# Kernel optimization log

Hardware: AMD Instinct MI355X
Metric: run time of the kernel (lower is better)

Reference implementation:

```python
import jax, jax.numpy as jnp
import numpy as np

N_NODES = 50000
N_EDGES = 800000


def setup_inputs() -> dict:
    key = jax.random.key(0)
    ks = jax.random.split(key, 8)
    return {
        "x": jax.random.normal(ks[0], (N_NODES, 256), dtype=jnp.float32),
        "adj_vals": jax.random.uniform(ks[1], (N_EDGES,), dtype=jnp.float32),
        "rows": jax.random.randint(ks[2], (N_EDGES,), 0, N_NODES, dtype=jnp.int32),
        "cols": jax.random.randint(ks[3], (N_EDGES,), 0, N_NODES, dtype=jnp.int32),
        "W1": jax.random.normal(ks[4], (256, 256), dtype=jnp.float32) * (1.0 / np.sqrt(256)),
        "b1": jnp.zeros((256,), dtype=jnp.float32),
        "W2": jax.random.normal(ks[5], (256, 256), dtype=jnp.float32) * (1.0 / np.sqrt(256)),
        "b2": jnp.zeros((256,), dtype=jnp.float32),
        "W3": jax.random.normal(ks[6], (256, 128), dtype=jnp.float32) * (1.0 / np.sqrt(256)),
        "b3": jnp.zeros((128,), dtype=jnp.float32),
    }


def reference(x, adj_vals, rows, cols, W1, b1, W2, b2, W3, b3):
    n = x.shape[0]

    def spmm(h):
        # sparse adjacency matmul: out[r] += val * h[c] over all edges (r, c)
        return jax.ops.segment_sum(adj_vals[:, None] * h[cols], rows, num_segments=n)

    # GCNLayer: adj @ (x @ W) + b ; ReLU between layers (dropout p=0 => identity)
    h = jax.nn.relu(spmm(x @ W1) + b1)
    h = jax.nn.relu(spmm(h @ W2) + b2)
    return spmm(h @ W3) + b3
```

## Files before the change

### kernel.cpp

```cpp
#include <hip/hip_runtime.h>
#include <hip/hip_bf16.h>


#define N_NODES 50000
#define N_EDGES 800000
#define KDIM 256
#define REP 8
#define NC (N_NODES * REP)
#define NB2 ((NC + 1023) / 1024)
#define NC_PAD (NB2 * 1024)

typedef __attribute__((ext_vector_type(8))) short short8;
typedef __attribute__((ext_vector_type(4))) float f32x4;

__device__ __forceinline__ ushort f2bf(float f) {
    union { float f; unsigned u; } x; x.f = f;
    unsigned r = x.u + 0x7fffu + ((x.u >> 16) & 1u);
    return (ushort)(r >> 16);
}
__device__ __forceinline__ float bf2f(ushort u) {
    union { unsigned u; float f; } x; x.u = ((unsigned)u) << 16;
    return x.f;
}

__global__ __launch_bounds__(256) void transpose_all_kernel(
        const float* __restrict__ W1, const float* __restrict__ W2,
        const float* __restrict__ W3, ushort* __restrict__ Wt1,
        ushort* __restrict__ Wt2, ushort* __restrict__ Wt3) {
    int id = blockIdx.x * blockDim.x + threadIdx.x;
    if (id < 65536) {
        int n = id >> 8, k = id & 255;
        Wt1[n * 256 + k] = f2bf(W1[k * 256 + n]);
    } else if (id < 131072) {
        int i = id - 65536, n = i >> 8, k = i & 255;
        Wt2[n * 256 + k] = f2bf(W2[k * 256 + n]);
    } else if (id < 163840) {
        int i = id - 131072, n = i >> 8, k = i & 255;
        Wt3[n * 256 + k] = f2bf(W3[k * 128 + n]);
    }
}


#define LDK 40

template <bool AFP32>
__device__ __forceinline__ void gemm_body(
        const void* __restrict__ Ain, const ushort* __restrict__ Wt,
        ushort* __restrict__ C, int M, int N, int bx, int by) {
    __shared__ ushort As[128 * LDK];
    __shared__ ushort Ws[128 * LDK];

    int t = threadIdx.x;
    int lane = t & 63;
    int w = t >> 6;
    int row0 = bx * 128, col0 = by * 128;
    int wm = (w & 1) * 64, wn = (w >> 1) * 64;
    int q = lane >> 4, mi = lane & 15;
    int r0 = t >> 2, kc = (t & 3) * 8;

    f32x4 acc[4][4];
    #pragma unroll
    for (int i = 0; i < 4; i++)
        #pragma unroll
        for (int j = 0; j < 4; j++) acc[i][j] = (f32x4)0.f;

    for (int k0 = 0; k0 < KDIM; k0 += 32) {
        int ga0 = row0 + r0;       if (ga0 >= M) ga0 = M - 1;
        int ga1 = row0 + r0 + 64;  if (ga1 >= M) ga1 = M - 1;
        short8 a0, a1;
        if (AFP32) {
            const float* Af = (const float*)Ain;
            float4 f0 = *(const float4*)&Af[ga0 * KDIM + k0 + kc];
            float4 f1 = *(const float4*)&Af[ga0 * KDIM + k0 + kc + 4];
            float4 f2 = *(const float4*)&Af[ga1 * KDIM + k0 + kc];
            float4 f3 = *(const float4*)&Af[ga1 * KDIM + k0 + kc + 4];
            a0[0] = (short)f2bf(f0.x); a0[1] = (short)f2bf(f0.y);
            a0[2] = (short)f2bf(f0.z); a0[3] = (short)f2bf(f0.w);
            a0[4] = (short)f2bf(f1.x); a0[5] = (short)f2bf(f1.y);
            a0[6] = (short)f2bf(f1.z); a0[7] = (short)f2bf(f1.w);
            a1[0] = (short)f2bf(f2.x); a1[1] = (short)f2bf(f2.y);
            a1[2] = (short)f2bf(f2.z); a1[3] = (short)f2bf(f2.w);
            a1[4] = (short)f2bf(f3.x); a1[5] = (short)f2bf(f3.y);
            a1[6] = (short)f2bf(f3.z); a1[7] = (short)f2bf(f3.w);
        } else {
            const ushort* Ab = (const ushort*)Ain;
            a0 = *(const short8*)&Ab[ga0 * KDIM + k0 + kc];
            a1 = *(const short8*)&Ab[ga1 * KDIM + k0 + kc];
        }
        short8 b0 = *(const short8*)&Wt[(col0 + r0) * KDIM + k0 + kc];
        short8 b1 = *(const short8*)&Wt[(col0 + r0 + 64) * KDIM + k0 + kc];
        __syncthreads();
        *(short8*)&As[r0 * LDK + kc]        = a0;
        *(short8*)&As[(r0 + 64) * LDK + kc] = a1;
        *(short8*)&Ws[r0 * LDK + kc]        = b0;
        *(short8*)&Ws[(r0 + 64) * LDK + kc] = b1;
        __syncthreads();

        short8 af[4], bf[4];
        #pragma unroll
        for (int mt = 0; mt < 4; mt++)
            af[mt] = *(const short8*)&As[(wm + mt * 16 + mi) * LDK + q * 8];
        #pragma unroll
        for (int nt = 0; nt < 4; nt++)
            bf[nt] = *(const short8*)&Ws[(wn + nt * 16 + mi) * LDK + q * 8];
        #pragma unroll
        for (int mt = 0; mt < 4; mt++)
            #pragma unroll
            for (int nt = 0; nt < 4; nt++)
                acc[mt][nt] = __builtin_amdgcn_mfma_f32_16x16x32_bf16(
                    af[mt], bf[nt], acc[mt][nt], 0, 0, 0);
    }

    #pragma unroll
    for (int mt = 0; mt < 4; mt++) {
        #pragma unroll
        for (int r = 0; r < 4; r++) {
            int grow = row0 + wm + mt * 16 + q * 4 + r;
            if (grow < M) {
                #pragma unroll
                for (int nt = 0; nt < 4; nt++) {
                    int gcol = col0 + wn + nt * 16 + mi;
                    C[grow * N + gcol] = f2bf(acc[mt][nt][r]);
                }
            }
        }
    }
}

#define GB1 782

__global__ __launch_bounds__(256) void gemm1_hist_kernel(
        const float* __restrict__ x, const ushort* __restrict__ Wt1,
        ushort* __restrict__ C, const int* __restrict__ rows,
        int* __restrict__ counts) {
    int b = blockIdx.x;
    if (b < GB1) {
        gemm_body<true>(x, Wt1, C, N_NODES, 256, b % 391, b / 391);
    } else {
        int e = (b - GB1) * 256 + threadIdx.x;
        if (e < N_EDGES) {
            int r = rows[e];
            atomicAdd(&counts[(r << 3) | (e & 7)], 1);
        }
    }
}

template <bool AFP32>
__global__ __launch_bounds__(256) void gemm_bf16_kernel(
        const void* __restrict__ Ain, const ushort* __restrict__ Wt,
        ushort* __restrict__ C, int M, int N) {
    gemm_body<AFP32>(Ain, Wt, C, M, N, blockIdx.x, blockIdx.y);
}


__global__ __launch_bounds__(256) void scan_sums(const int* __restrict__ counts,
                                                 int* __restrict__ bsum) {
    __shared__ int ws[4];
    int b = blockIdx.x, t = threadIdx.x, lane = t & 63, wv = t >> 6;
    int4 v = *(const int4*)&counts[b * 1024 + t * 4];
    int s = v.x + v.y + v.z + v.w;
    #pragma unroll
    for (int off = 32; off >= 1; off >>= 1) s += __shfl_down(s, off, 64);
    if (lane == 0) ws[wv] = s;
    __syncthreads();
    if (t == 0) bsum[b] = ws[0] + ws[1] + ws[2] + ws[3];
}

__global__ __launch_bounds__(512) void scan_block(const int* __restrict__ bsum,
                                                  int* __restrict__ boff,
                                                  int* __restrict__ rp8, int nb) {
    __shared__ int ws[8];
    int t = threadIdx.x, lane = t & 63, wv = t >> 6;
    int v = (t < nb) ? bsum[t] : 0;
    int incl = v;
    #pragma unroll
    for (int off = 1; off < 64; off <<= 1) {
        int u = __shfl_up(incl, off, 64);
        if (lane >= off) incl += u;
    }
    if (lane == 63) ws[wv] = incl;
    __syncthreads();
    int wo = 0;
    #pragma unroll
    for (int j = 0; j < 7; j++) wo += (j < wv) ? ws[j] : 0;
    if (t < nb) boff[t] = wo + incl - v;
    if (t == 511) rp8[NC] = wo + incl;
}

__global__ __launch_bounds__(256) void scan_apply(int* __restrict__ counts,
                                                  const int* __restrict__ boff,
                                                  int* __restrict__ rp8) {
    __shared__ int ws[4];
    int b = blockIdx.x, t = threadIdx.x, lane = t & 63, wv = t >> 6;
    int i = b * 1024 + t * 4;
    int4 v = *(const int4*)&counts[i];
    int s0 = v.x, s01 = s0 + v.y, s012 = s01 + v.z, tsum = s012 + v.w;
    int incl = tsum;
    #pragma unroll
    for (int off = 1; off < 64; off <<= 1) {
        int u = __shfl_up(incl, off, 64);
        if (lane >= off) incl += u;
    }
    if (lane == 63) ws[wv] = incl;
    __syncthreads();
    int woff = 0;
    #pragma unroll
    for (int j = 0; j < 3; j++) woff += (j < wv) ? ws[j] : 0;
    int base = boff[b] + woff + incl - tsum;
    if (i < NC)     rp8[i]     = base;
    if (i + 1 < NC) rp8[i + 1] = base + s0;
    if (i + 2 < NC) rp8[i + 2] = base + s01;
    if (i + 3 < NC) rp8[i + 3] = base + s012;
    *(int4*)&counts[i] = make_int4(0, 0, 0, 0);
}

__global__ void scatter_kernel(const int* __restrict__ rows, const int* __restrict__ cols,
                               const float* __restrict__ vals, const int* __restrict__ rp8,
                               int* __restrict__ counts, int2* __restrict__ cv) {
    int e = blockIdx.x * blockDim.x + threadIdx.x;
    if (e < N_EDGES) {
        int idx = (rows[e] << 3) | (e & 7);
        int pos = rp8[idx] + atomicAdd(&counts[idx], 1);
        cv[pos] = make_int2(cols[e], __float_as_int(vals[e]));
    }
}


template <int F, bool RELU, bool OUT_BF16>
__global__ __launch_bounds__(256) void spmm_kernel(
        const ushort* __restrict__ H, const int* __restrict__ rp8,
        const int2* __restrict__ cv, const float* __restrict__ bias,
        void* __restrict__ out, int nrows) {
    constexpr int FL = F / 8;
    constexpr int EP = 64 / FL;
    constexpr int STEP = EP * 4;
    int wave = threadIdx.x >> 6, lane = threadIdx.x & 63;
    int r = blockIdx.x * 4 + wave;
    if (r >= nrows) return;
    int fl = lane % FL, ep = lane / FL;
    const ushort* Hl = H + fl * 8;

    float acc[8];
    #pragma unroll
    for (int j = 0; j < 8; j++) acc[j] = 0.f;

    int start = rp8[r * REP], end = rp8[r * REP + REP];
    for (int base = start; base < end; base += STEP) {
        int e0 = base + ep * 4;
        int2 m0 = cv[e0], m1 = cv[e0 + 1], m2 = cv[e0 + 2], m3 = cv[e0 + 3];
        int   c0 = (e0     < end) ? m0.x : 0;
        int   c1 = (e0 + 1 < end) ? m1.x : 0;
        int   c2 = (e0 + 2 < end) ? m2.x : 0;
        int   c3 = (e0 + 3 < end) ? m3.x : 0;
        float v0 = (e0     < end) ? __int_as_float(m0.y) : 0.f;
        float v1 = (e0 + 1 < end) ? __int_as_float(m1.y) : 0.f;
        float v2 = (e0 + 2 < end) ? __int_as_float(m2.y) : 0.f;
        float v3 = (e0 + 3 < end) ? __int_as_float(m3.y) : 0.f;
        short8 h0 = *(const short8*)&Hl[(size_t)c0 * F];
        short8 h1 = *(const short8*)&Hl[(size_t)c1 * F];
        short8 h2 = *(const short8*)&Hl[(size_t)c2 * F];
        short8 h3 = *(const short8*)&Hl[(size_t)c3 * F];
        #pragma unroll
        for (int j = 0; j < 8; j++)
            acc[j] += v0 * bf2f((ushort)h0[j]) + v1 * bf2f((ushort)h1[j])
                    + v2 * bf2f((ushort)h2[j]) + v3 * bf2f((ushort)h3[j]);
    }

    #pragma unroll
    for (int off = FL; off < 64; off <<= 1)
        #pragma unroll
        for (int j = 0; j < 8; j++) acc[j] += __shfl_down(acc[j], off, 64);

    if (ep == 0) {
        #pragma unroll
        for (int j = 0; j < 8; j++) {
            float o = acc[j] + bias[fl * 8 + j];
            if (RELU) o = fmaxf(o, 0.f);
            acc[j] = o;
        }
        if (OUT_BF16) {
            short8 ob;
            #pragma unroll
            for (int j = 0; j < 8; j++) ob[j] = (short)f2bf(acc[j]);
            *(short8*)((ushort*)out + (size_t)r * F + fl * 8) = ob;
        } else {
            float* of = (float*)out + (size_t)r * F + fl * 8;
            *(float4*)&of[0] = make_float4(acc[0], acc[1], acc[2], acc[3]);
            *(float4*)&of[4] = make_float4(acc[4], acc[5], acc[6], acc[7]);
        }
    }
}


extern "C" void kernel_launch(void* const* d_in, const int* in_sizes, int n_in,
                              void* d_out, int out_size, void* d_ws, size_t ws_size,
                              hipStream_t stream) {
    const float* x    = (const float*)d_in[0];
    const float* av   = (const float*)d_in[1];
    const int*   rows = (const int*)d_in[2];
    const int*   cols = (const int*)d_in[3];
    const float* W1   = (const float*)d_in[4];
    const float* b1   = (const float*)d_in[5];
    const float* W2   = (const float*)d_in[6];
    const float* b2   = (const float*)d_in[7];
    const float* W3   = (const float*)d_in[8];
    const float* b3   = (const float*)d_in[9];
    float* out = (float*)d_out;

    const int N = N_NODES, E = N_EDGES;

    char* p = (char*)d_ws;
    auto carve = [&](size_t bytes) {
        void* q = (void*)p;
        p += (bytes + 255) & ~(size_t)255;
        return q;
    };
    ushort* bufG = (ushort*)carve((size_t)N * 256 * 2);
    ushort* bufH = (ushort*)carve((size_t)N * 256 * 2);
    ushort* Wt1  = (ushort*)carve((size_t)256 * 256 * 2);
    ushort* Wt2  = (ushort*)carve((size_t)256 * 256 * 2);
    ushort* Wt3  = (ushort*)carve((size_t)128 * 256 * 2);
    int*    rp8    = (int*)carve((size_t)(NC + 1) * 4);
    int*    counts = (int*)carve((size_t)NC_PAD * 4);
    int*    bsum   = (int*)carve((size_t)NB2 * 4);
    int*    boff   = (int*)carve((size_t)NB2 * 4);
    int2*   cv     = (int2*)carve((size_t)(E + 16) * 8);

    hipMemsetAsync(counts, 0, (size_t)NC_PAD * 4, stream);
    transpose_all_kernel<<<(163840 + 255) / 256, 256, 0, stream>>>(W1, W2, W3, Wt1, Wt2, Wt3);

    gemm1_hist_kernel<<<GB1 + (E + 255) / 256, 256, 0, stream>>>(x, Wt1, bufG, rows, counts);

    scan_sums<<<NB2, 256, 0, stream>>>(counts, bsum);
    scan_block<<<1, 512, 0, stream>>>(bsum, boff, rp8, NB2);
    scan_apply<<<NB2, 256, 0, stream>>>(counts, boff, rp8);
    scatter_kernel<<<(E + 255) / 256, 256, 0, stream>>>(rows, cols, av, rp8, counts, cv);

    int spmm_blocks = (N + 3) / 4;
    spmm_kernel<256, true, true><<<spmm_blocks, 256, 0, stream>>>(bufG, rp8, cv, b1, bufH, N);
    gemm_bf16_kernel<false><<<dim3(391, 2), 256, 0, stream>>>(bufH, Wt2, bufG, N, 256);
    spmm_kernel<256, true, true><<<spmm_blocks, 256, 0, stream>>>(bufG, rp8, cv, b2, bufH, N);
    gemm_bf16_kernel<false><<<dim3(391, 1), 256, 0, stream>>>(bufH, Wt3, bufG, N, 128);
    spmm_kernel<128, false, false><<<spmm_blocks, 256, 0, stream>>>(bufG, rp8, cv, b3, out, N);
}
```

Measured before the change: 373.2 us.

## Rewrite GEMM with full-K weight tile in LDS, prep kernel, wider SpMM unroll

Replaces the k-looped GEMM with a kernel that loads the whole 128x256 weight slice into swizzled LDS once and streams A fragments straight from global memory into MFMA, with each wave covering 64 rows by 128 columns. A new prep kernel casts x to bf16, builds the row histogram with vectorized atomics, and transposes the weights in one launch. The histogram replication factor goes from 8 to 16 to spread atomic contention, and the SpMM gathers 8 edges per lane instead of 4 for more memory-level parallelism. The trade-offs are an extra bf16 copy of x, no overlap of the first GEMM with the histogram, and higher register and LDS pressure (64 KB of LDS per block) in the GEMM.

New measurement: 395.8 us. 6.0% more time.

```diff
diff --git a/kernel.cpp b/kernel.cpp
--- a/kernel.cpp
+++ b/kernel.cpp
@@ -5,10 +5,14 @@
 #define N_NODES 50000
 #define N_EDGES 800000
 #define KDIM 256
-#define REP 8
+#define REP 16
 #define NC (N_NODES * REP)
 #define NB2 ((NC + 1023) / 1024)
 #define NC_PAD (NB2 * 1024)
+
+#define PB_CAST 6250
+#define PB_HIST 782
+#define PB_TR   640
 
 typedef __attribute__((ext_vector_type(8))) short short8;
 typedef __attribute__((ext_vector_type(4))) float f32x4;
@@ -23,133 +27,50 @@
     return x.f;
 }
 
-__global__ __launch_bounds__(256) void transpose_all_kernel(
+__global__ __launch_bounds__(256) void prep_kernel(
+        const float* __restrict__ x, ushort* __restrict__ xb,
+        const int* __restrict__ rows, int* __restrict__ counts,
         const float* __restrict__ W1, const float* __restrict__ W2,
         const float* __restrict__ W3, ushort* __restrict__ Wt1,
         ushort* __restrict__ Wt2, ushort* __restrict__ Wt3) {
-    int id = blockIdx.x * blockDim.x + threadIdx.x;
-    if (id < 65536) {
-        int n = id >> 8, k = id & 255;
-        Wt1[n * 256 + k] = f2bf(W1[k * 256 + n]);
-    } else if (id < 131072) {
-        int i = id - 65536, n = i >> 8, k = i & 255;
-        Wt2[n * 256 + k] = f2bf(W2[k * 256 + n]);
-    } else if (id < 163840) {
-        int i = id - 131072, n = i >> 8, k = i & 255;
-        Wt3[n * 256 + k] = f2bf(W3[k * 128 + n]);
-    }
-}
-
-
-#define LDK 40
-
-template <bool AFP32>
-__device__ __forceinline__ void gemm_body(
-        const void* __restrict__ Ain, const ushort* __restrict__ Wt,
-        ushort* __restrict__ C, int M, int N, int bx, int by) {
-    __shared__ ushort As[128 * LDK];
-    __shared__ ushort Ws[128 * LDK];
-
-    int t = threadIdx.x;
-    int lane = t & 63;
-    int w = t >> 6;
-    int row0 = bx * 128, col0 = by * 128;
-    int wm = (w & 1) * 64, wn = (w >> 1) * 64;
-    int q = lane >> 4, mi = lane & 15;
-    int r0 = t >> 2, kc = (t & 3) * 8;
-
-    f32x4 acc[4][4];
-    #pragma unroll
-    for (int i = 0; i < 4; i++)
-        #pragma unroll
-        for (int j = 0; j < 4; j++) acc[i][j] = (f32x4)0.f;
-
-    for (int k0 = 0; k0 < KDIM; k0 += 32) {
-        int ga0 = row0 + r0;       if (ga0 >= M) ga0 = M - 1;
-        int ga1 = row0 + r0 + 64;  if (ga1 >= M) ga1 = M - 1;
-        short8 a0, a1;
-        if (AFP32) {
-            const float* Af = (const float*)Ain;
-            float4 f0 = *(const float4*)&Af[ga0 * KDIM + k0 + kc];
-            float4 f1 = *(const float4*)&Af[ga0 * KDIM + k0 + kc + 4];
-            float4 f2 = *(const float4*)&Af[ga1 * KDIM + k0 + kc];
-            float4 f3 = *(const float4*)&Af[ga1 * KDIM + k0 + kc + 4];
-            a0[0] = (short)f2bf(f0.x); a0[1] = (short)f2bf(f0.y);
-            a0[2] = (short)f2bf(f0.z); a0[3] = (short)f2bf(f0.w);
-            a0[4] = (short)f2bf(f1.x); a0[5] = (short)f2bf(f1.y);
-            a0[6] = (short)f2bf(f1.z); a0[7] = (short)f2bf(f1.w);
-            a1[0] = (short)f2bf(f2.x); a1[1] = (short)f2bf(f2.y);
-            a1[2] = (short)f2bf(f2.z); a1[3] = (short)f2bf(f2.w);
-            a1[4] = (short)f2bf(f3.x); a1[5] = (short)f2bf(f3.y);
-            a1[6] = (short)f2bf(f3.z); a1[7] = (short)f2bf(f3.w);
+    int b = blockIdx.x, t = threadIdx.x;
+    if (b < PB_CAST) {
+        int i = (b * 256 + t) * 8;
+        float4 f0 = *(const float4*)&x[i];
+        float4 f1 = *(const float4*)&x[i + 4];
+        short8 o;
+        o[0] = (short)f2bf(f0.x); o[1] = (short)f2bf(f0.y);
+        o[2] = (short)f2bf(f0.z); o[3] = (short)f2bf(f0.w);
+        o[4] = (short)f2bf(f1.x); o[5] = (short)f2bf(f1.y);
+        o[6] = (short)f2bf(f1.z); o[7] = (short)f2bf(f1.w);
+        *(short8*)&xb[i] = o;
+    } else if (b < PB_CAST + PB_HIST) {
+        int e0 = (b - PB_CAST) * 1024 + t * 4;
+        if (e0 + 3 < N_EDGES) {
+            int4 r4 = *(const int4*)&rows[e0];
+            atomicAdd(&counts[(r4.x << 4) | ((e0    ) & 15)], 1);
+            atomicAdd(&counts[(r4.y << 4) | ((e0 + 1) & 15)], 1);
+            atomicAdd(&counts[(r4.z << 4) | ((e0 + 2) & 15)], 1);
+            atomicAdd(&counts[(r4.w << 4) | ((e0 + 3) & 15)], 1);
         } else {
-            const ushort* Ab = (const ushort*)Ain;
-            a0 = *(const short8*)&Ab[ga0 * KDIM + k0 + kc];
-            a1 = *(const short8*)&Ab[ga1 * KDIM + k0 + kc];
-        }
-        short8 b0 = *(const short8*)&Wt[(col0 + r0) * KDIM + k0 + kc];
-        short8 b1 = *(const short8*)&Wt[(col0 + r0 + 64) * KDIM + k0 + kc];
-        __syncthreads();
-        *(short8*)&As[r0 * LDK + kc]        = a0;
-        *(short8*)&As[(r0 + 64) * LDK + kc] = a1;
-        *(short8*)&Ws[r0 * LDK + kc]        = b0;
-        *(short8*)&Ws[(r0 + 64) * LDK + kc] = b1;
-        __syncthreads();
-
-        short8 af[4], bf[4];
-        #pragma unroll
-        for (int mt = 0; mt < 4; mt++)
-            af[mt] = *(const short8*)&As[(wm + mt * 16 + mi) * LDK + q * 8];
-        #pragma unroll
-        for (int nt = 0; nt < 4; nt++)
-            bf[nt] = *(const short8*)&Ws[(wn + nt * 16 + mi) * LDK + q * 8];
-        #pragma unroll
-        for (int mt = 0; mt < 4; mt++)
-            #pragma unroll
-            for (int nt = 0; nt < 4; nt++)
-                acc[mt][nt] = __builtin_amdgcn_mfma_f32_16x16x32_bf16(
-                    af[mt], bf[nt], acc[mt][nt], 0, 0, 0);
-    }
-
-    #pragma unroll
-    for (int mt = 0; mt < 4; mt++) {
-        #pragma unroll
-        for (int r = 0; r < 4; r++) {
-            int grow = row0 + wm + mt * 16 + q * 4 + r;
-            if (grow < M) {
-                #pragma unroll
-                for (int nt = 0; nt < 4; nt++) {
-                    int gcol = col0 + wn + nt * 16 + mi;
-                    C[grow * N + gcol] = f2bf(acc[mt][nt][r]);
-                }
+            for (int j = 0; j < 4; j++) {
+                int e = e0 + j;
+                if (e < N_EDGES) atomicAdd(&counts[(rows[e] << 4) | (e & 15)], 1);
             }
         }
-    }
-}
-
-#define GB1 782
-
-__global__ __launch_bounds__(256) void gemm1_hist_kernel(
-        const float* __restrict__ x, const ushort* __restrict__ Wt1,
-        ushort* __restrict__ C, const int* __restrict__ rows,
-        int* __restrict__ counts) {
-    int b = blockIdx.x;
-    if (b < GB1) {
-        gemm_body<true>(x, Wt1, C, N_NODES, 256, b % 391, b / 391);
     } else {
-        int e = (b - GB1) * 256 + threadIdx.x;
-        if (e < N_EDGES) {
-            int r = rows[e];
-            atomicAdd(&counts[(r << 3) | (e & 7)], 1);
-        }
-    }
-}
-
-template <bool AFP32>
-__global__ __launch_bounds__(256) void gemm_bf16_kernel(
-        const void* __restrict__ Ain, const ushort* __restrict__ Wt,
-        ushort* __restrict__ C, int M, int N) {
-    gemm_body<AFP32>(Ain, Wt, C, M, N, blockIdx.x, blockIdx.y);
+        int id = (b - PB_CAST - PB_HIST) * 256 + t;
+        if (id < 65536) {
+            int n = id >> 8, k = id & 255;
+            Wt1[n * 256 + k] = f2bf(W1[k * 256 + n]);
+        } else if (id < 131072) {
+            int i = id - 65536, n = i >> 8, k = i & 255;
+            Wt2[n * 256 + k] = f2bf(W2[k * 256 + n]);
+        } else {
+            int i = id - 131072, n = i >> 8, k = i & 255;
+            Wt3[n * 256 + k] = f2bf(W3[k * 128 + n]);
+        }
+    }
 }
 
 
@@ -166,10 +87,10 @@
     if (t == 0) bsum[b] = ws[0] + ws[1] + ws[2] + ws[3];
 }
 
-__global__ __launch_bounds__(512) void scan_block(const int* __restrict__ bsum,
-                                                  int* __restrict__ boff,
-                                                  int* __restrict__ rp8, int nb) {
-    __shared__ int ws[8];
+__global__ __launch_bounds__(1024) void scan_block(const int* __restrict__ bsum,
+                                                   int* __restrict__ boff,
+                                                   int* __restrict__ rp16, int nb) {
+    __shared__ int ws[16];
     int t = threadIdx.x, lane = t & 63, wv = t >> 6;
     int v = (t < nb) ? bsum[t] : 0;
     int incl = v;
@@ -182,14 +103,14 @@
     __syncthreads();
     int wo = 0;
     #pragma unroll
-    for (int j = 0; j < 7; j++) wo += (j < wv) ? ws[j] : 0;
+    for (int j = 0; j < 15; j++) wo += (j < wv) ? ws[j] : 0;
     if (t < nb) boff[t] = wo + incl - v;
-    if (t == 511) rp8[NC] = wo + incl;
+    if (t == 1023) rp16[NC] = wo + incl;
 }
 
 __global__ __launch_bounds__(256) void scan_apply(int* __restrict__ counts,
                                                   const int* __restrict__ boff,
-                                                  int* __restrict__ rp8) {
+                                                  int* __restrict__ rp16) {
     __shared__ int ws[4];
     int b = blockIdx.x, t = threadIdx.x, lane = t & 63, wv = t >> 6;
     int i = b * 1024 + t * 4;
@@ -207,33 +128,96 @@
     #pragma unroll
     for (int j = 0; j < 3; j++) woff += (j < wv) ? ws[j] : 0;
     int base = boff[b] + woff + incl - tsum;
-    if (i < NC)     rp8[i]     = base;
-    if (i + 1 < NC) rp8[i + 1] = base + s0;
-    if (i + 2 < NC) rp8[i + 2] = base + s01;
-    if (i + 3 < NC) rp8[i + 3] = base + s012;
+    if (i < NC)     rp16[i]     = base;
+    if (i + 1 < NC) rp16[i + 1] = base + s0;
+    if (i + 2 < NC) rp16[i + 2] = base + s01;
+    if (i + 3 < NC) rp16[i + 3] = base + s012;
     *(int4*)&counts[i] = make_int4(0, 0, 0, 0);
 }
 
 __global__ void scatter_kernel(const int* __restrict__ rows, const int* __restrict__ cols,
-                               const float* __restrict__ vals, const int* __restrict__ rp8,
+                               const float* __restrict__ vals, const int* __restrict__ rp16,
                                int* __restrict__ counts, int2* __restrict__ cv) {
     int e = blockIdx.x * blockDim.x + threadIdx.x;
     if (e < N_EDGES) {
-        int idx = (rows[e] << 3) | (e & 7);
-        int pos = rp8[idx] + atomicAdd(&counts[idx], 1);
+        int idx = (rows[e] << 4) | (e & 15);
+        int pos = rp16[idx] + atomicAdd(&counts[idx], 1);
         cv[pos] = make_int2(cols[e], __float_as_int(vals[e]));
+    }
+}
+
+
+__global__ __launch_bounds__(256) void gemm_kernel(
+        const ushort* __restrict__ A, const ushort* __restrict__ Wt,
+        ushort* __restrict__ C, int M, int N) {
+    __shared__ ushort Ws[128 * 256];
+
+    int t = threadIdx.x, lane = t & 63, w = t >> 6;
+    int row0 = blockIdx.x * 256 + w * 64;
+    int col0 = blockIdx.y * 128;
+    int q = lane >> 4, mi = lane & 15;
+
+    #pragma unroll
+    for (int i = 0; i < 16; i++) {
+        int u = i * 256 + t;
+        int c = u >> 5, ch = u & 31;
+        *(short8*)&Ws[c * 256 + (ch ^ (c & 31)) * 8] =
+            *(const short8*)&Wt[(col0 + c) * KDIM + ch * 8];
+    }
+    __syncthreads();
+
+    f32x4 acc[4][8];
+    #pragma unroll
+    for (int i = 0; i < 4; i++)
+        #pragma unroll
+        for (int j = 0; j < 8; j++) acc[i][j] = (f32x4)0.f;
+
+    #pragma unroll
+    for (int ks = 0; ks < 8; ks++) {
+        int kc = ks * 4 + q;
+        short8 af[4], bf[8];
+        #pragma unroll
+        for (int mt = 0; mt < 4; mt++) {
+            int gr = row0 + mt * 16 + mi;
+            if (gr >= M) gr = M - 1;
+            af[mt] = *(const short8*)&A[gr * KDIM + kc * 8];
+        }
+        #pragma unroll
+        for (int nt = 0; nt < 8; nt++) {
+            int cc = nt * 16 + mi;
+            bf[nt] = *(const short8*)&Ws[cc * 256 + (kc ^ (cc & 31)) * 8];
+        }
+        #pragma unroll
+        for (int mt = 0; mt < 4; mt++)
+            #pragma unroll
+            for (int nt = 0; nt < 8; nt++)
+                acc[mt][nt] = __builtin_amdgcn_mfma_f32_16x16x32_bf16(
+                    af[mt], bf[nt], acc[mt][nt], 0, 0, 0);
+    }
+
+    #pragma unroll
+    for (int mt = 0; mt < 4; mt++) {
+        #pragma unroll
+        for (int r = 0; r < 4; r++) {
+            int grow = row0 + mt * 16 + q * 4 + r;
+            if (grow < M) {
+                #pragma unroll
+                for (int nt = 0; nt < 8; nt++)
+                    C[grow * N + col0 + nt * 16 + mi] = f2bf(acc[mt][nt][r]);
+            }
+        }
     }
 }
 
 
 template <int F, bool RELU, bool OUT_BF16>
 __global__ __launch_bounds__(256) void spmm_kernel(
-        const ushort* __restrict__ H, const int* __restrict__ rp8,
+        const ushort* __restrict__ H, const int* __restrict__ rp16,
         const int2* __restrict__ cv, const float* __restrict__ bias,
         void* __restrict__ out, int nrows) {
     constexpr int FL = F / 8;
     constexpr int EP = 64 / FL;
-    constexpr int STEP = EP * 4;
+    constexpr int STEP = EP * 8;
     int wave = threadIdx.x >> 6, lane = threadIdx.x & 63;
     int r = blockIdx.x * 4 + wave;
     if (r >= nrows) return;
@@ -244,26 +228,27 @@
     #pragma unroll
     for (int j = 0; j < 8; j++) acc[j] = 0.f;
 
-    int start = rp8[r * REP], end = rp8[r * REP + REP];
+    int start = rp16[r * REP], end = rp16[r * REP + REP];
     for (int base = start; base < end; base += STEP) {
-        int e0 = base + ep * 4;
-        int2 m0 = cv[e0], m1 = cv[e0 + 1], m2 = cv[e0 + 2], m3 = cv[e0 + 3];
-        int   c0 = (e0     < end) ? m0.x : 0;
-        int   c1 = (e0 + 1 < end) ? m1.x : 0;
-        int   c2 = (e0 + 2 < end) ? m2.x : 0;
-        int   c3 = (e0 + 3 < end) ? m3.x : 0;
-        float v0 = (e0     < end) ? __int_as_float(m0.y) : 0.f;
-        float v1 = (e0 + 1 < end) ? __int_as_float(m1.y) : 0.f;
-        float v2 = (e0 + 2 < end) ? __int_as_float(m2.y) : 0.f;
-        float v3 = (e0 + 3 < end) ? __int_as_float(m3.y) : 0.f;
-        short8 h0 = *(const short8*)&Hl[(size_t)c0 * F];
-        short8 h1 = *(const short8*)&Hl[(size_t)c1 * F];
-        short8 h2 = *(const short8*)&Hl[(size_t)c2 * F];
-        short8 h3 = *(const short8*)&Hl[(size_t)c3 * F];
-        #pragma unroll
-        for (int j = 0; j < 8; j++)
-            acc[j] += v0 * bf2f((ushort)h0[j]) + v1 * bf2f((ushort)h1[j])
-                    + v2 * bf2f((ushort)h2[j]) + v3 * bf2f((ushort)h3[j]);
+        int e0 = base + ep * 8;
+        int2 m[8];
+        #pragma unroll
+        for (int i = 0; i < 8; i++) m[i] = cv[e0 + i];
+        int c[8]; float v[8];
+        #pragma unroll
+        for (int i = 0; i < 8; i++) {
+            bool p = (e0 + i) < end;
+            c[i] = p ? m[i].x : 0;
+            v[i] = p ? __int_as_float(m[i].y) : 0.f;
+        }
+        short8 h[8];
+        #pragma unroll
+        for (int i = 0; i < 8; i++) h[i] = *(const short8*)&Hl[(size_t)c[i] * F];
+        #pragma unroll
+        for (int i = 0; i < 8; i++)
+            #pragma unroll
+            for (int j = 0; j < 8; j++)
+                acc[j] += v[i] * bf2f((ushort)h[i][j]);
     }
 
     #pragma unroll
@@ -315,31 +300,35 @@
         p += (bytes + 255) & ~(size_t)255;
         return q;
     };
+    ushort* xb   = (ushort*)carve((size_t)N * 256 * 2);
     ushort* bufG = (ushort*)carve((size_t)N * 256 * 2);
     ushort* bufH = (ushort*)carve((size_t)N * 256 * 2);
     ushort* Wt1  = (ushort*)carve((size_t)256 * 256 * 2);
     ushort* Wt2  = (ushort*)carve((size_t)256 * 256 * 2);
     ushort* Wt3  = (ushort*)carve((size_t)128 * 256 * 2);
-    int*    rp8    = (int*)carve((size_t)(NC + 1) * 4);
+    int*    rp16   = (int*)carve((size_t)(NC + 1) * 4);
     int*    counts = (int*)carve((size_t)NC_PAD * 4);
     int*    bsum   = (int*)carve((size_t)NB2 * 4);
     int*    boff   = (int*)carve((size_t)NB2 * 4);
-    int2*   cv     = (int2*)carve((size_t)(E + 16) * 8);
+    int2*   cv     = (int2*)carve((size_t)(E + 64) * 8);
 
     hipMemsetAsync(counts, 0, (size_t)NC_PAD * 4, stream);
-    transpose_all_kernel<<<(163840 + 255) / 256, 256, 0, stream>>>(W1, W2, W3, Wt1, Wt2, Wt3);
-
-    gemm1_hist_kernel<<<GB1 + (E + 255) / 256, 256, 0, stream>>>(x, Wt1, bufG, rows, counts);
+    prep_kernel<<<PB_CAST + PB_HIST + PB_TR, 256, 0, stream>>>(
+        x, xb, rows, counts, W1, W2, W3, Wt1, Wt2, Wt3);
 
     scan_sums<<<NB2, 256, 0, stream>>>(counts, bsum);
-    scan_block<<<1, 512, 0, stream>>>(bsum, boff, rp8, NB2);
-    scan_apply<<<NB2, 256, 0, stream>>>(counts, boff, rp8);
-    scatter_kernel<<<(E + 255) / 256, 256, 0, stream>>>(rows, cols, av, rp8, counts, cv);
-
+    scan_block<<<1, 1024, 0, stream>>>(bsum, boff, rp16, NB2);
+    scan_apply<<<NB2, 256, 0, stream>>>(counts, boff, rp16);
+    scatter_kernel<<<(E + 255) / 256, 256, 0, stream>>>(rows, cols, av, rp16, counts, cv);
+
+    dim3 g2((N + 255) / 256, 2);
+    dim3 g1((N + 255) / 256, 1);
     int spmm_blocks = (N + 3) / 4;
-    spmm_kernel<256, true, true><<<spmm_blocks, 256, 0, stream>>>(bufG, rp8, cv, b1, bufH, N);
-    gemm_bf16_kernel<false><<<dim3(391, 2), 256, 0, stream>>>(bufH, Wt2, bufG, N, 256);
-    spmm_kernel<256, true, true><<<spmm_blocks, 256, 0, stream>>>(bufG, rp8, cv, b2, bufH, N);
-    gemm_bf16_kernel<false><<<dim3(391, 1), 256, 0, stream>>>(bufH, Wt3, bufG, N, 128);
-    spmm_kernel<128, false, false><<<spmm_blocks, 256, 0, stream>>>(bufG, rp8, cv, b3, out, N);
-}
+
+    gemm_kernel<<<g2, 256, 0, stream>>>(xb, Wt1, bufG, N, 256);
+    spmm_kernel<256, true, true><<<spmm_blocks, 256, 0, stream>>>(bufG, rp16, cv, b1, bufH, N);
+    gemm_kernel<<<g2, 256, 0, stream>>>(bufH, Wt2, bufG, N, 256);
+    spmm_kernel<256, true, true><<<spmm_blocks, 256, 0, stream>>>(bufG, rp16, cv, b2, bufH, N);
+    gemm_kernel<<<g1, 256, 0, stream>>>(bufH, Wt3, bufG, N, 128);
+    spmm_kernel<128, false, false><<<spmm_blocks, 256, 0, stream>>>(bufG, rp16, cv, b3, out, N);
+}
```
